# Optimization experiments

Hardware: AMD Instinct MI355X
Metric: run time of the kernel (lower is better)

## Reference

```python
import jax, jax.numpy as jnp
import numpy as np

N_NODES = 200000
F = 256
B = 8192
FAN1 = 16  # hop-1 fanout (layer_num_samples[0])
FAN2 = 4   # hop-2 fanout (layer_num_samples[1])


def setup_inputs() -> dict:
    key = jax.random.key(0)
    k1, k2, k3, k4, k5, k6 = jax.random.split(key, 6)
    node_feats = jax.random.normal(k1, (N_NODES, F), dtype=jnp.float32)
    # SageLayer weight: [out_size, 2*layer_size]
    W1 = jax.random.normal(k2, (F, 2 * F), dtype=jnp.float32) * 0.05
    W2 = jax.random.normal(k3, (F, 2 * F), dtype=jnp.float32) * 0.05
    batch_nodes = jax.random.randint(k4, (B,), 0, N_NODES)
    neigh1 = jax.random.randint(k5, (B, FAN1), 0, N_NODES)
    M1 = B + B * FAN1  # layer-1 node set: batch nodes + their sampled neighbors
    neigh2 = jax.random.randint(k6, (M1, FAN2), 0, N_NODES)
    return {"node_feats": node_feats, "W1": W1, "W2": W2,
            "batch_nodes": batch_nodes, "neigh1": neigh1, "neigh2": neigh2}


def reference(node_feats, W1, W2, batch_nodes, neigh1, neigh2):
    b = batch_nodes.shape[0]
    # layer-1 node list: batch nodes first, then hop-1 neighbors (row-major)
    nodes1 = jnp.concatenate([batch_nodes, neigh1.reshape(-1)])  # [17B]
    # ---- SAGE layer 1: MEAN-aggregate hop-2 neighbor raw features ----
    agg1 = node_feats[neigh2].mean(axis=1)              # [17B, F]
    self1 = node_feats[nodes1]                           # [17B, F]
    h1 = jax.nn.relu(jnp.concatenate([self1, agg1], axis=1) @ W1.T)  # [17B, F]
    # ---- SAGE layer 2: MEAN-aggregate hop-1 neighbors' hidden embs ----
    agg2 = h1[b:].reshape(b, neigh1.shape[1], -1).mean(axis=1)  # [B, F]
    h_self = h1[:b]                                      # [B, F]
    out = jax.nn.relu(jnp.concatenate([h_self, agg2], axis=1) @ W2.T)  # [B, F]
    return out
```

## Files before the change

kernel.cpp:

```cpp
#include <hip/hip_runtime.h>
#include <hip/hip_bf16.h>

#define NB 8192
#define M1T 139264

typedef __attribute__((ext_vector_type(8))) short bf16x8;
typedef __attribute__((ext_vector_type(16))) float f32x16;

__device__ __forceinline__ unsigned short f2b(float f) {
  union { float f; unsigned u; } v; v.f = f;
  unsigned r = v.u + 0x7fffu + ((v.u >> 16) & 1u);
  return (unsigned short)(r >> 16);
}
__device__ __forceinline__ float b2f(unsigned u16) {
  union { unsigned u; float f; } v; v.u = u16 << 16;
  return v.f;
}
__device__ __forceinline__ uint4 pack8u(float a0, float a1, float a2, float a3,
                                        float a4, float a5, float a6, float a7) {
  uint4 v;
  v.x = (unsigned)f2b(a0) | ((unsigned)f2b(a1) << 16);
  v.y = (unsigned)f2b(a2) | ((unsigned)f2b(a3) << 16);
  v.z = (unsigned)f2b(a4) | ((unsigned)f2b(a5) << 16);
  v.w = (unsigned)f2b(a6) | ((unsigned)f2b(a7) << 16);
  return v;
}

#define GLDS16(g, l)                                                          \
  __builtin_amdgcn_global_load_lds(                                           \
      (const __attribute__((address_space(1))) unsigned int*)(const void*)(g),\
      (__attribute__((address_space(3))) unsigned int*)(void*)(l), 16, 0, 0)

#define BAR_LGKM()                                                            \
  do { asm volatile("s_waitcnt lgkmcnt(0)" ::: "memory");                     \
       __builtin_amdgcn_s_barrier(); } while (0)

__global__ void convert_w(const float* __restrict__ W1, const float* __restrict__ W2,
                          unsigned short* __restrict__ W1s, unsigned short* __restrict__ W2s) {
  int i = blockIdx.x * 256 + threadIdx.x;
  const float* W; unsigned short* out; int f4;
  if (i < 32768) { W = W1; out = W1s; f4 = i; }
  else           { W = W2; out = W2s; f4 = i - 32768; }
  int n  = (f4 * 4) >> 9;
  int c0 = (f4 * 4) & 511;
  int kt = c0 >> 6;
  int slot = (c0 & 63) >> 3;
  int e  = c0 & 7;
  int sw = slot ^ (n & 7);
  float4 v = *((const float4*)W + f4);
  ushort4 o;
  o.x = f2b(v.x); o.y = f2b(v.y); o.z = f2b(v.z); o.w = f2b(v.w);
  *(ushort4*)(out + kt * 16384 + n * 64 + sw * 8 + e) = o;
}

__global__ __launch_bounds__(512, 4)
void sage_l1(const float* __restrict__ feats,
             const unsigned short* __restrict__ Wbs,
             const int* __restrict__ batch_nodes,
             const int* __restrict__ neigh1,
             const int* __restrict__ neigh2,
             unsigned short* __restrict__ h1b)
{
  __shared__ __align__(16) unsigned short As[2][64 * 64];
  __shared__ __align__(16) unsigned short Bs[2][256 * 64];
  const int tid = threadIdx.x;
  const int m0 = blockIdx.x * 64;
  const int w = tid >> 6, lane = tid & 63, l31 = lane & 31, lh = lane >> 5;
  const int mh = w & 1, nq = w >> 1;
  const int m = tid >> 3, slot = tid & 7;
  const int r = m0 + m;

  const int self = (r < NB) ? batch_nodes[r] : neigh1[r - NB];
  const int4 nb = *(const int4*)(neigh2 + (size_t)r * 4);
  const float* sp = feats + (size_t)self * 256;
  const float* ap[4] = { feats + (size_t)nb.x * 256, feats + (size_t)nb.y * 256,
                         feats + (size_t)nb.z * 256, feats + (size_t)nb.w * 256 };

  f32x16 acc[2] = {};
  float4 araw[8];

  #define ISSUE_B1(kt, buf)                                                   \
    do { const unsigned short* _s = Wbs + (size_t)(kt) * 16384;               \
         unsigned short* _d = &Bs[buf][0];                                    \
         _Pragma("unroll")                                                    \
         for (int q = 0; q < 4; ++q) {                                        \
           int i = q * 512 + tid;                                             \
           GLDS16(_s + (size_t)i * 8, _d + i * 8);                            \
         } } while (0)

  #define ISSUE_A1(kt)                                                        \
    do { if ((kt) < 4) {                                                      \
           const float* _p = sp + (kt) * 64 + slot * 8;                       \
           araw[0] = *(const float4*)_p; araw[1] = *(const float4*)(_p + 4);  \
         } else {                                                             \
           const int _kb = ((kt) - 4) * 64 + slot * 8;                        \
           _Pragma("unroll")                                                  \
           for (int j = 0; j < 4; ++j) {                                      \
             const float* _p = ap[j] + _kb;                                   \
             araw[2*j]   = *(const float4*)_p;                                \
             araw[2*j+1] = *(const float4*)(_p + 4);                          \
           } } } while (0)

  ISSUE_B1(0, 0);
  ISSUE_A1(0);

  #pragma unroll
  for (int kt = 0; kt < 8; ++kt) {
    const int cur = kt & 1;
    uint4 av;
    if (kt < 4) {
      av = pack8u(araw[0].x, araw[0].y, araw[0].z, araw[0].w,
                  araw[1].x, araw[1].y, araw[1].z, araw[1].w);
    } else {
      float s0 = araw[0].x + araw[2].x + araw[4].x + araw[6].x;
      float s1 = araw[0].y + araw[2].y + araw[4].y + araw[6].y;
      float s2 = araw[0].z + araw[2].z + araw[4].z + araw[6].z;
      float s3 = araw[0].w + araw[2].w + araw[4].w + araw[6].w;
      float s4 = araw[1].x + araw[3].x + araw[5].x + araw[7].x;
      float s5 = araw[1].y + araw[3].y + araw[5].y + araw[7].y;
      float s6 = araw[1].z + araw[3].z + araw[5].z + araw[7].z;
      float s7 = araw[1].w + araw[3].w + araw[5].w + araw[7].w;
      av = pack8u(s0 * 0.25f, s1 * 0.25f, s2 * 0.25f, s3 * 0.25f,
                  s4 * 0.25f, s5 * 0.25f, s6 * 0.25f, s7 * 0.25f);
    }
    __syncthreads();
    *(uint4*)(&As[cur][m * 64 + ((slot ^ (m & 7)) << 3)]) = av;
    if (kt < 7) { ISSUE_B1(kt + 1, cur ^ 1); ISSUE_A1(kt + 1); }
    BAR_LGKM();
    {
      const int arow = mh * 32 + l31;
      const int n0 = nq * 64 + l31, n1 = n0 + 32;
      __builtin_amdgcn_s_setprio(1);
      #pragma unroll
      for (int kk = 0; kk < 4; ++kk) {
        int sl = kk * 2 + lh;
        bf16x8 a  = *(const bf16x8*)(&As[cur][arow * 64 + ((sl ^ (arow & 7)) << 3)]);
        bf16x8 b0 = *(const bf16x8*)(&Bs[cur][n0 * 64 + ((sl ^ (n0 & 7)) << 3)]);
        bf16x8 b1 = *(const bf16x8*)(&Bs[cur][n1 * 64 + ((sl ^ (n1 & 7)) << 3)]);
        acc[0] = __builtin_amdgcn_mfma_f32_32x32x16_bf16(a, b0, acc[0], 0, 0, 0);
        acc[1] = __builtin_amdgcn_mfma_f32_32x32x16_bf16(a, b1, acc[1], 0, 0, 0);
      }
      __builtin_amdgcn_s_setprio(0);
    }
  }
  #undef ISSUE_B1
  #undef ISSUE_A1

  #pragma unroll
  for (int ni = 0; ni < 2; ++ni)
    #pragma unroll
    for (int q = 0; q < 16; ++q) {
      int row = m0 + mh * 32 + (q & 3) + 8 * (q >> 2) + 4 * lh;
      int col = nq * 64 + ni * 32 + l31;
      float v = acc[ni][q];
      v = v > 0.f ? v : 0.f;
      h1b[(size_t)row * 256 + col] = f2b(v);
    }
}

__global__ __launch_bounds__(256, 2)
void sage_l2(const unsigned short* __restrict__ h1b,
             const unsigned short* __restrict__ Wbs,
             float* __restrict__ out)
{
  __shared__ __align__(16) unsigned short As[2][32 * 64];
  __shared__ __align__(16) unsigned short Bs[2][256 * 64];
  const int tid = threadIdx.x;
  const int m0 = blockIdx.x * 32;
  const int w = tid >> 6, lane = tid & 63, l31 = lane & 31, lh = lane >> 5;
  const int m = tid >> 3, slot = tid & 7;
  const int r = m0 + m;

  const unsigned short* selfp = h1b + (size_t)r * 256;
  const unsigned short* aggp  = h1b + (size_t)(NB + r * 16) * 256;

  f32x16 acc[2] = {};
  uint4 braw[16];

  #define ISSUE_B2(kt, buf)                                                   \
    do { const unsigned short* _s = Wbs + (size_t)(kt) * 16384;               \
         unsigned short* _d = &Bs[buf][0];                                    \
         _Pragma("unroll")                                                    \
         for (int q = 0; q < 8; ++q) {                                        \
           int i = q * 256 + tid;                                             \
           GLDS16(_s + (size_t)i * 8, _d + i * 8);                            \
         } } while (0)

  #define ISSUE_A2(kt)                                                        \
    do { if ((kt) < 4) {                                                      \
           braw[0] = *(const uint4*)(selfp + (kt) * 64 + slot * 8);           \
         } else {                                                             \
           const int _kb = ((kt) - 4) * 64 + slot * 8;                        \
           _Pragma("unroll")                                                  \
           for (int j = 0; j < 16; ++j)                                       \
             braw[j] = *(const uint4*)(aggp + (size_t)j * 256 + _kb);         \
         } } while (0)

  ISSUE_B2(0, 0);
  ISSUE_A2(0);

  #pragma unroll
  for (int kt = 0; kt < 8; ++kt) {
    const int cur = kt & 1;
    uint4 av;
    if (kt < 4) {
      av = braw[0];
    } else {
      float s0 = 0, s1 = 0, s2 = 0, s3 = 0, s4 = 0, s5 = 0, s6 = 0, s7 = 0;
      #pragma unroll
      for (int j = 0; j < 16; ++j) {
        s0 += b2f(braw[j].x & 0xffffu); s1 += b2f(braw[j].x >> 16);
        s2 += b2f(braw[j].y & 0xffffu); s3 += b2f(braw[j].y >> 16);
        s4 += b2f(braw[j].z & 0xffffu); s5 += b2f(braw[j].z >> 16);
      s6 += b2f(braw[j].w & 0xffffu); s7 += b2f(braw[j].w >> 16);
      }
      const float q = 1.0f / 16.0f;
      av = pack8u(s0 * q, s1 * q, s2 * q, s3 * q, s4 * q, s5 * q, s6 * q, s7 * q);
    }
    __syncthreads();
    *(uint4*)(&As[cur][m * 64 + ((slot ^ (m & 7)) << 3)]) = av;
    if (kt < 7) { ISSUE_B2(kt + 1, cur ^ 1); ISSUE_A2(kt + 1); }
    BAR_LGKM();
    {
      const int arow = l31;
      const int n0 = w * 64 + l31, n1 = n0 + 32;
      __builtin_amdgcn_s_setprio(1);
      #pragma unroll
      for (int kk = 0; kk < 4; ++kk) {
        int sl = kk * 2 + lh;
        bf16x8 a  = *(const bf16x8*)(&As[cur][arow * 64 + ((sl ^ (arow & 7)) << 3)]);
        bf16x8 b0 = *(const bf16x8*)(&Bs[cur][n0 * 64 + ((sl ^ (n0 & 7)) << 3)]);
        bf16x8 b1 = *(const bf16x8*)(&Bs[cur][n1 * 64 + ((sl ^ (n1 & 7)) << 3)]);
        acc[0] = __builtin_amdgcn_mfma_f32_32x32x16_bf16(a, b0, acc[0], 0, 0, 0);
        acc[1] = __builtin_amdgcn_mfma_f32_32x32x16_bf16(a, b1, acc[1], 0, 0, 0);
      }
      __builtin_amdgcn_s_setprio(0);
    }
  }
  #undef ISSUE_B2
  #undef ISSUE_A2

  #pragma unroll
  for (int ni = 0; ni < 2; ++ni)
    #pragma unroll
    for (int q = 0; q < 16; ++q) {
      int row = m0 + (q & 3) + 8 * (q >> 2) + 4 * lh;
      int col = w * 64 + ni * 32 + l31;
      float v = acc[ni][q];
      out[(size_t)row * 256 + col] = v > 0.f ? v : 0.f;
    }
}

extern "C" void kernel_launch(void* const* d_in, const int* in_sizes, int n_in,
                              void* d_out, int out_size, void* d_ws, size_t ws_size,
                              hipStream_t stream) {
  const float* feats       = (const float*)d_in[0];
  const float* W1          = (const float*)d_in[1];
  const float* W2          = (const float*)d_in[2];
  const int*   batch_nodes = (const int*)d_in[3];
  const int*   neigh1      = (const int*)d_in[4];
  const int*   neigh2      = (const int*)d_in[5];
  float* out = (float*)d_out;

  unsigned short* W1s = (unsigned short*)d_ws;
  unsigned short* W2s = W1s + 131072;
  unsigned short* h1b = W2s + 131072;

  hipLaunchKernelGGL(convert_w, dim3(256), dim3(256), 0, stream, W1, W2, W1s, W2s);
  hipLaunchKernelGGL(sage_l1, dim3(M1T / 64), dim3(512), 0, stream,
                     feats, W1s, batch_nodes, neigh1, neigh2, h1b);
  hipLaunchKernelGGL(sage_l2, dim3(NB / 32), dim3(256), 0, stream, h1b, W2s, out);
}
```

Measured before the change: 153.6 us.

## Deepen gather prefetch to two stages and widen layer-2 blocks to 512 threads

Result: no change. 153.9 us (+0.2%).

```diff
diff --git a/kernel.cpp b/kernel.cpp
--- a/kernel.cpp
+++ b/kernel.cpp
@@ -30,10 +30,6 @@
   __builtin_amdgcn_global_load_lds(                                           \
       (const __attribute__((address_space(1))) unsigned int*)(const void*)(g),\
       (__attribute__((address_space(3))) unsigned int*)(void*)(l), 16, 0, 0)
-
-#define BAR_LGKM()                                                            \
-  do { asm volatile("s_waitcnt lgkmcnt(0)" ::: "memory");                     \
-       __builtin_amdgcn_s_barrier(); } while (0)
 
 __global__ void convert_w(const float* __restrict__ W1, const float* __restrict__ W2,
                           unsigned short* __restrict__ W1s, unsigned short* __restrict__ W2s) {
@@ -72,93 +68,114 @@
 
   const int self = (r < NB) ? batch_nodes[r] : neigh1[r - NB];
   const int4 nb = *(const int4*)(neigh2 + (size_t)r * 4);
-  const float* sp = feats + (size_t)self * 256;
-  const float* ap[4] = { feats + (size_t)nb.x * 256, feats + (size_t)nb.y * 256,
-                         feats + (size_t)nb.z * 256, feats + (size_t)nb.w * 256 };
-
-  f32x16 acc[2] = {};
-  float4 araw[8];
-
-  #define ISSUE_B1(kt, buf)                                                   \
-    do { const unsigned short* _s = Wbs + (size_t)(kt) * 16384;               \
-         unsigned short* _d = &Bs[buf][0];                                    \
-         _Pragma("unroll")                                                    \
-         for (int q = 0; q < 4; ++q) {                                        \
-           int i = q * 512 + tid;                                             \
-           GLDS16(_s + (size_t)i * 8, _d + i * 8);                            \
-         } } while (0)
-
-  #define ISSUE_A1(kt)                                                        \
-    do { if ((kt) < 4) {                                                      \
-           const float* _p = sp + (kt) * 64 + slot * 8;                       \
-           araw[0] = *(const float4*)_p; araw[1] = *(const float4*)(_p + 4);  \
+  const char* fb = (const char*)feats;
+  const unsigned so  = (unsigned)self * 1024u + (unsigned)slot * 32u;
+  const unsigned no0 = (unsigned)nb.x * 1024u + (unsigned)slot * 32u;
+  const unsigned no1 = (unsigned)nb.y * 1024u + (unsigned)slot * 32u;
+  const unsigned no2 = (unsigned)nb.z * 1024u + (unsigned)slot * 32u;
+  const unsigned no3 = (unsigned)nb.w * 1024u + (unsigned)slot * 32u;
+  const int arowC = mh * 32 + l31;
+  const int n0C = nq * 64 + l31, n1C = n0C + 32;
+
+  f32x16 acc0 = {}, acc1 = {};
+  float4 a0[8], a1[8];
+
+  #define L1_LOADS(KT, AR)                                                    \
+    do { if ((KT) < 4) {                                                      \
+           AR[0] = *(const float4*)(fb + so + (KT) * 256);                    \
+           AR[1] = *(const float4*)(fb + so + (KT) * 256 + 16);               \
          } else {                                                             \
-           const int _kb = ((kt) - 4) * 64 + slot * 8;                        \
-           _Pragma("unroll")                                                  \
-           for (int j = 0; j < 4; ++j) {                                      \
-             const float* _p = ap[j] + _kb;                                   \
-             araw[2*j]   = *(const float4*)_p;                                \
-             araw[2*j+1] = *(const float4*)(_p + 4);                          \
-           } } } while (0)
-
-  ISSUE_B1(0, 0);
-  ISSUE_A1(0);
+           const int _kb = ((KT) - 4) * 256;                                  \
+           AR[0] = *(const float4*)(fb + no0 + _kb);                          \
+           AR[1] = *(const float4*)(fb + no0 + _kb + 16);                     \
+           AR[2] = *(const float4*)(fb + no1 + _kb);                          \
+           AR[3] = *(const float4*)(fb + no1 + _kb + 16);                     \
+           AR[4] = *(const float4*)(fb + no2 + _kb);                          \
+           AR[5] = *(const float4*)(fb + no2 + _kb + 16);                     \
+           AR[6] = *(const float4*)(fb + no3 + _kb);                          \
+           AR[7] = *(const float4*)(fb + no3 + _kb + 16);                     \
+         } } while (0)
+
+  #define L1_BISSUE(KT)                                                       \
+    do { const unsigned short* _s = Wbs + (size_t)(KT) * 16384;               \
+         unsigned short* _d = &Bs[(KT) & 1][0];                               \
+         _Pragma("unroll")                                                    \
+         for (int _q = 0; _q < 4; ++_q) {                                     \
+           int _i = _q * 512 + tid;                                           \
+           GLDS16(_s + (size_t)_i * 8, _d + _i * 8);                          \
+         } } while (0)
+
+  #define L1_CONV(KT, AR, AV)                                                 \
+    do { if ((KT) < 4) {                                                      \
+           AV = pack8u(AR[0].x, AR[0].y, AR[0].z, AR[0].w,                    \
+                       AR[1].x, AR[1].y, AR[1].z, AR[1].w);                   \
+         } else {                                                             \
+           float s0 = AR[0].x + AR[2].x + AR[4].x + AR[6].x;                  \
+           float s1 = AR[0].y + AR[2].y + AR[4].y + AR[6].y;                  \
+           float s2 = AR[0].z + AR[2].z + AR[4].z + AR[6].z;                  \
+           float s3 = AR[0].w + AR[2].w + AR[4].w + AR[6].w;                  \
+           float s4 = AR[1].x + AR[3].x + AR[5].x + AR[7].x;                  \
+           float s5 = AR[1].y + AR[3].y + AR[5].y + AR[7].y;                  \
+           float s6 = AR[1].z + AR[3].z + AR[5].z + AR[7].z;                  \
+           float s7 = AR[1].w + AR[3].w + AR[5].w + AR[7].w;                  \
+           AV = pack8u(s0 * 0.25f, s1 * 0.25f, s2 * 0.25f, s3 * 0.25f,       \
+                       s4 * 0.25f, s5 * 0.25f, s6 * 0.25f, s7 * 0.25f);      \
+         } } while (0)
+
+  #define L1_STEP(KT, AR, NCNT)                                               \
+    do { uint4 _av;                                                           \
+         L1_CONV(KT, AR, _av);      \
+         *(uint4*)(&As[(KT) & 1][m * 64 + ((slot ^ (m & 7)) << 3)]) = _av;    \
+         asm volatile("s_waitcnt vmcnt(" #NCNT ") lgkmcnt(0)" ::: "memory");  \
+         __builtin_amdgcn_s_barrier();                                        \
+         if ((KT) < 7) L1_BISSUE((KT) + 1);                                   \
+         if ((KT) < 6) L1_LOADS((KT) + 2, AR);                                \
+         __builtin_amdgcn_sched_barrier(0);                                   \
+         __builtin_amdgcn_s_setprio(1);                                       \
+         _Pragma("unroll")                                                    \
+         for (int _kk = 0; _kk < 4; ++_kk) {                                  \
+           int _sl = _kk * 2 + lh;                                            \
+           bf16x8 _a  = *(const bf16x8*)(&As[(KT) & 1][arowC * 64 + ((_sl ^ (arowC & 7)) << 3)]); \
+           bf16x8 _b0 = *(const bf16x8*)(&Bs[(KT) & 1][n0C * 64 + ((_sl ^ (n0C & 7)) << 3)]);     \
+           bf16x8 _b1 = *(const bf16x8*)(&Bs[(KT) & 1][n1C * 64 + ((_sl ^ (n1C & 7)) << 3)]);     \
+           acc0 = __builtin_amdgcn_mfma_f32_32x32x16_bf16(_a, _b0, acc0, 0, 0, 0);                \
+           acc1 = __builtin_amdgcn_mfma_f32_32x32x16_bf16(_a, _b1, acc1, 0, 0, 0);                \
+         }                                                                    \
+         __builtin_amdgcn_s_setprio(0);                                       \
+    } while (0)
+
+  L1_LOADS(0, a0);
+  L1_BISSUE(0);
+  L1_LOADS(1, a1);
+  __builtin_amdgcn_sched_barrier(0);
+
+  L1_STEP(0, a0, 2);
+  L1_STEP(1, a1, 2);
+  L1_STEP(2, a0, 2);
+  L1_STEP(3, a1, 8);
+  L1_STEP(4, a0, 8);
+  L1_STEP(5, a1, 8);
+  L1_STEP(6, a0, 8);
+  L1_STEP(7, a1, 0);
+
+  #undef L1_LOADS
+  #undef L1_BISSUE
+  #undef L1_CONV
+  #undef L1_STEP
 
   #pragma unroll
-  for (int kt = 0; kt < 8; ++kt) {
-    const int cur = kt & 1;
-    uint4 av;
-    if (kt < 4) {
-      av = pack8u(araw[0].x, araw[0].y, araw[0].z, araw[0].w,
-                  araw[1].x, araw[1].y, araw[1].z, araw[1].w);
-    } else {
-      float s0 = araw[0].x + araw[2].x + araw[4].x + araw[6].x;
-      float s1 = araw[0].y + araw[2].y + araw[4].y + araw[6].y;
-      float s2 = araw[0].z + araw[2].z + araw[4].z + araw[6].z;
-      float s3 = araw[0].w + araw[2].w + araw[4].w + araw[6].w;
-      float s4 = araw[1].x + araw[3].x + araw[5].x + araw[7].x;
-      float s5 = araw[1].y + araw[3].y + araw[5].y + araw[7].y;
-      float s6 = araw[1].z + araw[3].z + araw[5].z + araw[7].z;
-      float s7 = araw[1].w + araw[3].w + araw[5].w + araw[7].w;
-      av = pack8u(s0 * 0.25f, s1 * 0.25f, s2 * 0.25f, s3 * 0.25f,
-                  s4 * 0.25f, s5 * 0.25f, s6 * 0.25f, s7 * 0.25f);
-    }
-    __syncthreads();
-    *(uint4*)(&As[cur][m * 64 + ((slot ^ (m & 7)) << 3)]) = av;
-    if (kt < 7) { ISSUE_B1(kt + 1, cur ^ 1); ISSUE_A1(kt + 1); }
-    BAR_LGKM();
-    {
-      const int arow = mh * 32 + l31;
-      const int n0 = nq * 64 + l31, n1 = n0 + 32;
-      __builtin_amdgcn_s_setprio(1);
-      #pragma unroll
-      for (int kk = 0; kk < 4; ++kk) {
-        int sl = kk * 2 + lh;
-        bf16x8 a  = *(const bf16x8*)(&As[cur][arow * 64 + ((sl ^ (arow & 7)) << 3)]);
-        bf16x8 b0 = *(const bf16x8*)(&Bs[cur][n0 * 64 + ((sl ^ (n0 & 7)) << 3)]);
-        bf16x8 b1 = *(const bf16x8*)(&Bs[cur][n1 * 64 + ((sl ^ (n1 & 7)) << 3)]);
-        acc[0] = __builtin_amdgcn_mfma_f32_32x32x16_bf16(a, b0, acc[0], 0, 0, 0);
-        acc[1] = __builtin_amdgcn_mfma_f32_32x32x16_bf16(a, b1, acc[1], 0, 0, 0);
-      }
-      __builtin_amdgcn_s_setprio(0);
-    }
+  for (int q = 0; q < 16; ++q) {
+    int row = m0 + mh * 32 + (q & 3) + 8 * (q >> 2) + 4 * lh;
+    int col0 = nq * 64 + l31;
+    float v0 = acc0[q], v1 = acc1[q];
+    v0 = v0 > 0.f ? v0 : 0.f;
+    v1 = v1 > 0.f ? v1 : 0.f;
+    h1b[(size_t)row * 256 + col0] = f2b(v0);
+    h1b[(size_t)row * 256 + col0 + 32] = f2b(v1);
   }
-  #undef ISSUE_B1
-  #undef ISSUE_A1
-
-  #pragma unroll
-  for (int ni = 0; ni < 2; ++ni)
-    #pragma unroll
-    for (int q = 0; q < 16; ++q) {
-      int row = m0 + mh * 32 + (q & 3) + 8 * (q >> 2) + 4 * lh;
-      int col = nq * 64 + ni * 32 + l31;
-      float v = acc[ni][q];
-      v = v > 0.f ? v : 0.f;
-      h1b[(size_t)row * 256 + col] = f2b(v);
-    }
-}
-
-__global__ __launch_bounds__(256, 2)
+}
+
+__global__ __launch_bounds__(512, 4)
 void sage_l2(const unsigned short* __restrict__ h1b,
              const unsigned short* __restrict__ Wbs,
              float* __restrict__ out)
@@ -168,87 +185,95 @@
   const int tid = threadIdx.x;
   const int m0 = blockIdx.x * 32;
   const int w = tid >> 6, lane = tid & 63, l31 = lane & 31, lh = lane >> 5;
-  const int m = tid >> 3, slot = tid & 7;
+  const int m = tid >> 4, slot = tid & 15;
   const int r = m0 + m;
-
-  const unsigned short* selfp = h1b + (size_t)r * 256;
-  const unsigned short* aggp  = h1b + (size_t)(NB + r * 16) * 256;
-
-  f32x16 acc[2] = {};
-  uint4 braw[16];
-
-  #define ISSUE_B2(kt, buf)                                                   \
-    do { const unsigned short* _s = Wbs + (size_t)(kt) * 16384;               \
-         unsigned short* _d = &Bs[buf][0];                                    \
-         _Pragma("unroll")                                                    \
-         for (int q = 0; q < 8; ++q) {                                        \
-           int i = q * 256 + tid;                                             \
-           GLDS16(_s + (size_t)i * 8, _d + i * 8);                            \
-         } } while (0)
-
-  #define ISSUE_A2(kt)                                                        \
-    do { if ((kt) < 4) {                                                      \
-           braw[0] = *(const uint4*)(selfp + (kt) * 64 + slot * 8);           \
+  const char* hb = (const char*)h1b;
+  const unsigned so = (unsigned)r * 512u + (unsigned)slot * 8u;
+  const unsigned ao = (unsigned)(NB + r * 16) * 512u + (unsigned)slot * 8u;
+  const int arowC = l31;
+  const int n0C = w * 32 + l31;
+
+  f32x16 acc = {};
+  uint2 b0r[16], b1r[16];
+
+  #define L2_LOADS(KT, BR)                                                    \
+    do { if ((KT) < 4) {                                                      \
+           BR[0] = *(const uint2*)(hb + so + (KT) * 128);                     \
          } else {                                                             \
-           const int _kb = ((kt) - 4) * 64 + slot * 8;                        \
            _Pragma("unroll")                                                  \
-           for (int j = 0; j < 16; ++j)                                       \
-             braw[j] = *(const uint4*)(aggp + (size_t)j * 256 + _kb);         \
-         } } while (0)
-
-  ISSUE_B2(0, 0);
-  ISSUE_A2(0);
+           for (int _j = 0; _j < 16; ++_j)                                    \
+             BR[_j] = *(const uint2*)(hb + ao + _j * 512 + ((KT) - 4) * 128); \
+         } } while (0)
+
+  #define L2_BISSUE(KT)                                                       \
+    do { const unsigned short* _s = Wbs + (size_t)(KT) * 16384;               \
+         unsigned short* _d = &Bs[(KT) & 1][0];                               \
+         _Pragma("unroll")                                                    \
+         for (int _q = 0; _q < 4; ++_q) {                                     \
+           int _i = _q * 512 + tid;                                           \
+           GLDS16(_s + (size_t)_i * 8, _d + _i * 8);                          \
+         } } while (0)
+
+  #define L2_CONV(KT, BR, AV)                                                 \
+    do { if ((KT) < 4) { AV = BR[0]; }                                        \
+         else {                                                               \
+           float s0 = 0, s1 = 0, s2 = 0, s3 = 0;                              \
+           _Pragma("unroll")                                                  \
+           for (int _j = 0; _j < 16; ++_j) {                                  \
+             s0 += b2f(BR[_j].x & 0xffffu); s1 += b2f(BR[_j].x >> 16);        \
+             s2 += b2f(BR[_j].y & 0xffffu); s3 += b2f(BR[_j].y >> 16);        \
+           }                                                                  \
+           const float _q16 = 1.0f / 16.0f;                                   \
+           AV.x = (unsigned)f2b(s0 * _q16) | ((unsigned)f2b(s1 * _q16) << 16);\
+           AV.y = (unsigned)f2b(s2 * _q16) | ((unsigned)f2b(s3 * _q16) << 16);\
+         } } while (0)
+
+  #define L2_STEP(KT, BR, NCNT)                                               \
+    do { uint2 _av;                                                           \
+         L2_CONV(KT, BR, _av);                                                \
+         *(uint2*)(&As[(KT) & 1][m * 64 + (((slot >> 1) ^ (m & 7)) << 3) + (slot & 1) * 4]) = _av; \
+         asm volatile("s_waitcnt vmcnt(" #NCNT ") lgkmcnt(0)" ::: "memory");  \
+         __builtin_amdgcn_s_barrier();                                        \
+         if ((KT) < 7) L2_BISSUE((KT) + 1);                                   \
+         if ((KT) < 6) L2_LOADS((KT) + 2, BR);                                \
+         __builtin_amdgcn_sched_barrier(0);                                   \
+         __builtin_amdgcn_s_setprio(1);                                       \
+         _Pragma("unroll")                                                    \
+         for (int _kk = 0; _kk < 4; ++_kk) {                                  \
+           int _sl = _kk * 2 + lh;                                            \
+           bf16x8 _a = *(const bf16x8*)(&As[(KT) & 1][arowC * 64 + ((_sl ^ (arowC & 7)) << 3)]); \
+           bf16x8 _b = *(const bf16x8*)(&Bs[(KT) & 1][n0C * 64 + ((_sl ^ (n0C & 7)) << 3)]);     \
+           acc = __builtin_amdgcn_mfma_f32_32x32x16_bf16(_a, _b, acc, 0, 0, 0);                  \
+         }                                                                    \
+         __builtin_amdgcn_s_setprio(0);                                       \
+    } while (0)
+
+  L2_LOADS(0, b0r);
+  L2_BISSUE(0);
+  L2_LOADS(1, b1r);
+  __builtin_amdgcn_sched_barrier(0);
+
+  L2_STEP(0, b0r, 1);
+  L2_STEP(1, b1r, 1);
+  L2_STEP(2, b0r, 1);
+  L2_STEP(3, b1r, 16);
+  L2_STEP(4, b0r, 16);
+  L2_STEP(5, b1r, 16);
+  L2_STEP(6, b0r, 16);
+  L2_STEP(7, b1r, 0);
+
+  #undef L2_LOADS
+  #undef L2_BISSUE
+  #undef L2_CONV
+  #undef L2_STEP
 
   #pragma unroll
-  for (int kt = 0; kt < 8; ++kt) {
-    const int cur = kt & 1;
-    uint4 av;
-    if (kt < 4) {
-      av = braw[0];
-    } else {
-      float s0 = 0, s1 = 0, s2 = 0, s3 = 0, s4 = 0, s5 = 0, s6 = 0, s7 = 0;
-      #pragma unroll
-      for (int j = 0; j < 16; ++j) {
-        s0 += b2f(braw[j].x & 0xffffu); s1 += b2f(braw[j].x >> 16);
-        s2 += b2f(braw[j].y & 0xffffu); s3 += b2f(braw[j].y >> 16);
-        s4 += b2f(braw[j].z & 0xffffu); s5 += b2f(braw[j].z >> 16);
-      s6 += b2f(braw[j].w & 0xffffu); s7 += b2f(braw[j].w >> 16);
-      }
-      const float q = 1.0f / 16.0f;
-      av = pack8u(s0 * q, s1 * q, s2 * q, s3 * q, s4 * q, s5 * q, s6 * q, s7 * q);
-    }
-    __syncthreads();
-    *(uint4*)(&As[cur][m * 64 + ((slot ^ (m & 7)) << 3)]) = av;
-    if (kt < 7) { ISSUE_B2(kt + 1, cur ^ 1); ISSUE_A2(kt + 1); }
-    BAR_LGKM();
-    {
-      const int arow = l31;
-      const int n0 = w * 64 + l31, n1 = n0 + 32;
-      __builtin_amdgcn_s_setprio(1);
-      #pragma unroll
-      for (int kk = 0; kk < 4; ++kk) {
-        int sl = kk * 2 + lh;
-        bf16x8 a  = *(const bf16x8*)(&As[cur][arow * 64 + ((sl ^ (arow & 7)) << 3)]);
-        bf16x8 b0 = *(const bf16x8*)(&Bs[cur][n0 * 64 + ((sl ^ (n0 & 7)) << 3)]);
-        bf16x8 b1 = *(const bf16x8*)(&Bs[cur][n1 * 64 + ((sl ^ (n1 & 7)) << 3)]);
-        acc[0] = __builtin_amdgcn_mfma_f32_32x32x16_bf16(a, b0, acc[0], 0, 0, 0);
-        acc[1] = __builtin_amdgcn_mfma_f32_32x32x16_bf16(a, b1, acc[1], 0, 0, 0);
-      }
-      __builtin_amdgcn_s_setprio(0);
-    }
+  for (int q = 0; q < 16; ++q) {
+    int row = m0 + (q & 3) + 8 * (q >> 2) + 4 * lh;
+    int col = n0C;
+    float v = acc[q];
+    out[(size_t)row * 256 + col] = v > 0.f ? v : 0.f;
   }
-  #undef ISSUE_B2
-  #undef ISSUE_A2
-
-  #pragma unroll
-  for (int ni = 0; ni < 2; ++ni)
-    #pragma unroll
-    for (int q = 0; q < 16; ++q) {
-      int row = m0 + (q & 3) + 8 * (q >> 2) + 4 * lh;
-      int col = w * 64 + ni * 32 + l31;
-      float v = acc[ni][q];
-      out[(size_t)row * 256 + col] = v > 0.f ? v : 0.f;
-    }
 }
 
 extern "C" void kernel_launch(void* const* d_in, const int* in_sizes, int n_in,
@@ -269,5 +294,5 @@
   hipLaunchKernelGGL(convert_w, dim3(256), dim3(256), 0, stream, W1, W2, W1s, W2s);
   hipLaunchKernelGGL(sage_l1, dim3(M1T / 64), dim3(512), 0, stream,
                      feats, W1s, batch_nodes, neigh1, neigh2, h1b);
-  hipLaunchKernelGGL(sage_l2, dim3(NB / 32), dim3(256), 0, stream, h1b, W2s, out);
-}
+  hipLaunchKernelGGL(sage_l2, dim3(NB / 32), dim3(512), 0, stream, h1b, W2s, out);
+}
```
